# Optimization experiments

Hardware: AMD Instinct MI355X
Metric: run time of the kernel (lower is better)

The kernel has to match this reference:

```python
import jax, jax.numpy as jnp
import numpy as np


def setup_inputs() -> dict:
    key = jax.random.key(0)
    k1, k2, k3 = jax.random.split(key, 3)
    p = 4096
    target = jax.random.normal(k1, (p, p), dtype=jnp.float32)
    source = jax.random.normal(k2, (p, p), dtype=jnp.float32)
    W_beta = jax.random.uniform(k3, (p, p), dtype=jnp.float32)
    return {"target": target, "source": source, "W_beta": W_beta}


def reference(target, source, W_beta):
    # X = target, Y = source (module-level names in the original).
    # denominator inner loop: sum_i X[i] . X[i] == ||X||_F^2 (scalar),
    # recomputed p^2 times in the original; computed once here.
    s = jnp.sum(target * target)
    W = W_beta.sum(axis=1)                       # [p]
    W2 = W * W                                   # [p]
    scale = W2 / (s * W2 + 1.0)                  # [p]
    G = jnp.matmul(source, target.T)             # [p,p], G[i,j] = Y[i] . X[j]
    W_matrix = scale[:, None] * G                # [p,p]
    primary = jnp.matmul(W_matrix, target) - source
    loss = jnp.sqrt(jnp.sum(jnp.square(jnp.matmul(W_beta, primary))))
    return loss, W_matrix
```

## Files before the change

### kernel.cpp

```cpp
#include <hip/hip_runtime.h>
#include <hip/hip_bf16.h>

#define PDIM 4096
#define PPN ((size_t)PDIM * (size_t)PDIM)

typedef __attribute__((ext_vector_type(8))) short bf16x8;
typedef __attribute__((ext_vector_type(4))) float floatx4;
typedef __attribute__((ext_vector_type(8))) int int8v;

__device__ __forceinline__ void load_lds16(const void* g, void* l) {
  __builtin_amdgcn_global_load_lds(
      (const __attribute__((address_space(1))) void*)g,
      (__attribute__((address_space(3))) void*)l, 16, 0, 0);
}

__device__ __forceinline__ unsigned short bf16bits(float f) {
  __hip_bfloat16 h = __float2bfloat16(f);
  return *(unsigned short*)&h;
}

__device__ __forceinline__ unsigned char fp8byte(float v) {
  return (unsigned char)(__builtin_amdgcn_cvt_pk_fp8_f32(v, v, 0, false) & 0xff);
}
__device__ __forceinline__ unsigned int fp8x4(float a, float b, float c, float d) {
  int v = __builtin_amdgcn_cvt_pk_fp8_f32(a, b, 0, false);
  v = __builtin_amdgcn_cvt_pk_fp8_f32(c, d, v, true);
  return (unsigned int)v;
}

__global__ void sumsq(const float4* __restrict__ x, float* __restrict__ acc) {
  float s = 0.f;
  const size_t n4 = PPN / 4;
  for (size_t i = (size_t)blockIdx.x * 256 + threadIdx.x; i < n4;
       i += (size_t)gridDim.x * 256) {
    const float4 v = x[i];
    s += v.x * v.x + v.y * v.y + v.z * v.z + v.w * v.w;
  }
#pragma unroll
  for (int off = 32; off > 0; off >>= 1) s += __shfl_down(s, off);
  __shared__ float ws[4];
  if ((threadIdx.x & 63) == 0) ws[threadIdx.x >> 6] = s;
  __syncthreads();
  if (threadIdx.x == 0) atomicAdd(acc, ws[0] + ws[1] + ws[2] + ws[3]);
}

__global__ void cast_x(const float* __restrict__ src,
                       __hip_bfloat16* __restrict__ dstN,
                       unsigned char* __restrict__ dstT8) {
  __shared__ float tile[64][65];
  const int bx = blockIdx.x * 64, by = blockIdx.y * 64;
  const int tx = threadIdx.x & 15, ty = threadIdx.x >> 4;
#pragma unroll
  for (int r = 0; r < 4; ++r) {
    const int row = ty + r * 16;
    const float4 v = *(const float4*)&src[(size_t)(by + row) * PDIM + bx + tx * 4];
    tile[row][tx * 4 + 0] = v.x;
    tile[row][tx * 4 + 1] = v.y;
    tile[row][tx * 4 + 2] = v.z;
    tile[row][tx * 4 + 3] = v.w;
    ushort4 o;
    o.x = bf16bits(v.x); o.y = bf16bits(v.y); o.z = bf16bits(v.z); o.w = bf16bits(v.w);
    *(ushort4*)&dstN[(size_t)(by + row) * PDIM + bx + tx * 4] = o;
  }
  __syncthreads();
#pragma unroll
  for (int r = 0; r < 4; ++r) {
    const int i = ty + r * 16;
    *(unsigned int*)&dstT8[(size_t)(bx + i) * PDIM + by + tx * 4] =
        fp8x4(tile[tx * 4 + 0][i], tile[tx * 4 + 1][i],
              tile[tx * 4 + 2][i], tile[tx * 4 + 3][i]);
  }
}

__global__ void cast_y(const float* __restrict__ src,
                       __hip_bfloat16* __restrict__ dstN,
                       __hip_bfloat16* __restrict__ dstT) {
  __shared__ float tile[64][65];
  const int bx = blockIdx.x * 64, by = blockIdx.y * 64;
  const int tx = threadIdx.x & 15, ty = threadIdx.x >> 4;
#pragma unroll
  for (int r = 0; r < 4; ++r) {
    const int row = ty + r * 16;
    const float4 v = *(const float4*)&src[(size_t)(by + row) * PDIM + bx + tx * 4];
    tile[row][tx * 4 + 0] = v.x;
    tile[row][tx * 4 + 1] = v.y;
    tile[row][tx * 4 + 2] = v.z;
    tile[row][tx * 4 + 3] = v.w;
    ushort4 o;
    o.x = bf16bits(v.x); o.y = bf16bits(v.y); o.z = bf16bits(v.z); o.w = bf16bits(v.w);
    *(ushort4*)&dstN[(size_t)(by + row) * PDIM + bx + tx * 4] = o;
  }
  __syncthreads();
#pragma unroll
  for (int r = 0; r < 4; ++r) {
    const int i = ty + r * 16;
    ushort4 o;
    o.x = bf16bits(tile[tx * 4 + 0][i]);
    o.y = bf16bits(tile[tx * 4 + 1][i]);
    o.z = bf16bits(tile[tx * 4 + 2][i]);
    o.w = bf16bits(tile[tx * 4 + 3][i]);
    *(ushort4*)&dstT[(size_t)(bx + i) * PDIM + by + tx * 4] = o;
  }
}

__global__ void cast_wb_rows(const float* __restrict__ Wb,
                             unsigned char* __restrict__ Wb8,
                             const float* __restrict__ sAcc,
                             float* __restrict__ scale) {
  const size_t row = blockIdx.x;
  const float4* src = (const float4*)(Wb + row * PDIM);
  unsigned int* dst = (unsigned int*)(Wb8 + row * PDIM);
  float sum = 0.f;
#pragma unroll
  for (int it = 0; it < 4; ++it) {
    const int j = threadIdx.x + it * 256;
    const float4 v = src[j];
    sum += (v.x + v.y) + (v.z + v.w);
    dst[j] = fp8x4(v.x, v.y, v.z, v.w);
  }
#pragma unroll
  for (int off = 32; off > 0; off >>= 1) sum += __shfl_down(sum, off);
  __shared__ float ws[4];
  if ((threadIdx.x & 63) == 0) ws[threadIdx.x >> 6] = sum;
  __syncthreads();
  if (threadIdx.x == 0) {
    const float W = ws[0] + ws[1] + ws[2] + ws[3];
    const float w2 = W * W;
    scale[row] = w2 / ((*sAcc) * w2 + 1.0f);
  }
}

__global__ __launch_bounds__(256)
void gemm_bf16_wm(const __hip_bfloat16* __restrict__ A,
                  const __hip_bfloat16* __restrict__ B,
                  const float* __restrict__ scale,
                  float* __restrict__ outF,
                  unsigned char* __restrict__ Wm8) {
  __shared__ __align__(16) __hip_bfloat16 As[128 * 32];
  __shared__ __align__(16) __hip_bfloat16 Bs[128 * 32];

  const int tid = threadIdx.x;
  const int lane = tid & 63;
  const int wave = tid >> 6;
  const int wm = wave >> 1, wn = wave & 1;

  const size_t rowA0 = (size_t)blockIdx.y * 128;
  const size_t rowB0 = (size_t)blockIdx.x * 128;

  const int c0 = tid, c1 = tid + 256;
  const int r0 = c0 >> 2, r1 = c1 >> 2;
  const int sc0 = (c0 & 3) ^ ((r0 >> 1) & 3);
  const int sc1 = (c1 & 3) ^ ((r1 >> 1) & 3);
  const __hip_bfloat16* gA0 = A + (rowA0 + (size_t)r0) * PDIM + sc0 * 8;
  const __hip_bfloat16* gA1 = A + (rowA0 + (size_t)r1) * PDIM + sc1 * 8;
  const __hip_bfloat16* gB0 = B + (rowB0 + (size_t)r0) * PDIM + sc0 * 8;
  const __hip_bfloat16* gB1 = B + (rowB0 + (size_t)r1) * PDIM + sc1 * 8;

  char* ldsA0 = (char*)As + wave * 1024;
  char* ldsA1 = (char*)As + 4096 + wave * 1024;
  char* ldsB0 = (char*)Bs + wave * 1024;
  char* ldsB1 = (char*)Bs + 4096 + wave * 1024;

  floatx4 acc[4][4] = {};

  const int fr = lane & 15;
  const int kq = lane >> 4;
  const int sw = (fr >> 1) & 3;
  const int ko = (kq ^ sw) * 16;

  for (int kt = 0; kt < PDIM; kt += 32) {
    load_lds16(gA0 + kt, ldsA0);
    load_lds16(gA1 + kt, ldsA1);
    load_lds16(gB0 + kt, ldsB0);
    load_lds16(gB1 + kt, ldsB1);
    __syncthreads();

    bf16x8 af[4], bfr[4];
#pragma unroll
    for (int mi = 0; mi < 4; ++mi)
      af[mi] = *(const bf16x8*)((const char*)As + (wm * 64 + mi * 16 + fr) * 64 + ko);
#pragma unroll
    for (int ni = 0; ni < 4; ++ni)
      bfr[ni] = *(const bf16x8*)((const char*)Bs + (wn * 64 + ni * 16 + fr) * 64 + ko);
#pragma unroll
    for (int mi = 0; mi < 4; ++mi)
#pragma unroll
      for (int ni = 0; ni < 4; ++ni)
        acc[mi][ni] = __builtin_amdgcn_mfma_f32_16x16x32_bf16(
            af[mi], bfr[ni], acc[mi][ni], 0, 0, 0);
    __syncthreads();
  }

  const size_t row0 = rowA0 + wm * 64;
  const size_t col0 = rowB0 + wn * 64;
  const int lr = (lane >> 4) << 2;
  const int lc = lane & 15;

#pragma unroll
  for (int mi = 0; mi < 4; ++mi) {
#pragma unroll
    for (int r = 0; r < 4; ++r) {
      const size_t row = row0 + mi * 16 + lr + r;
      const float sc = scale[row];
#pragma unroll
      for (int ni = 0; ni < 4; ++ni) {
        const size_t col = col0 + ni * 16 + lc;
        const float v = sc * acc[mi][ni][r];
        outF[row * PDIM + col] = v;
        Wm8[row * PDIM + col] = fp8byte(v * 131072.f);
      }
    }
  }
}

template <int MODE>
__global__ __launch_bounds__(256)
void gemm_fp8(const unsigned char* __restrict__ A,
              const unsigned char* __restrict__ B,
              const __hip_bfloat16* __restrict__ sub,
              unsigned char* __restrict__ outP,
              float* __restrict__ lossAcc) {
  __shared__ __align__(16) unsigned char As[128 * 128];
  __shared__ __align__(16) unsigned char Bs[128 * 128];

  const int tid = threadIdx.x;
  const int lane = tid & 63;
  const int wave = tid >> 6;
  const int wm = wave >> 1, wn = wave & 1;

  const size_t rowA0 = (size_t)blockIdx.y * 128;
  const size_t rowB0 = (size_t)blockIdx.x * 128;

  const unsigned char* gA[4];
  const unsigned char* gB[4];
  int ldsOff[4];
#pragma unroll
  for (int m = 0; m < 4; ++m) {
    const int ci = tid + m * 256;
    const int r = ci >> 3, s = ci & 7;
    const int cg = s ^ (r & 7);
    gA[m] = A + (rowA0 + (size_t)r) * PDIM + cg * 16;
    gB[m] = B + (rowB0 + (size_t)r) * PDIM + cg * 16;
    ldsOff[m] = m * 4096 + wave * 1024;
  }

  floatx4 acc[4][4] = {};

  const int fr = lane & 15;
  const int e = fr & 7;
  const int q2 = (lane >> 4) << 1;
  const int offLo = (q2 ^ e) << 4;
  const int offHi = ((q2 + 1) ^ e) << 4;
  const int abase = (wm * 64 + fr) * 128;
  const int bbase = (wn * 64 + fr) * 128;

  for (int kt = 0; kt < PDIM; kt += 128) {
#pragma unroll
    for (int m = 0; m < 4; ++m) load_lds16(gA[m] + kt, (char*)As + ldsOff[m]);
#pragma unroll
    for (int m = 0; m < 4; ++m) load_lds16(gB[m] + kt, (char*)Bs + ldsOff[m]);
    __syncthreads();

    union { int8v v; int4 h[2]; } af[4], bg[4];
#pragma unroll
    for (int mi = 0; mi < 4; ++mi) {
      af[mi].h[0] = *(const int4*)(As + abase + mi * 2048 + offLo);
      af[mi].h[1] = *(const int4*)(As + abase + mi * 2048 + offHi);
    }
#pragma unroll
    for (int ni = 0; ni < 4; ++ni) {
      bg[ni].h[0] = *(const int4*)(Bs + bbase + ni * 2048 + offLo);
      bg[ni].h[1] = *(const int4*)(Bs + bbase + ni * 2048 + offHi);
    }
#pragma unroll
    for (int mi = 0; mi < 4; ++mi)
#pragma unroll
      for (int ni = 0; ni < 4; ++ni)
        acc[mi][ni] = __builtin_amdgcn_mfma_scale_f32_16x16x128_f8f6f4(
            af[mi].v, bg[ni].v, acc[mi][ni],
            0 , 0 , 0, 0x7F7F7F7F, 0, 0x7F7F7F7F);
    __syncthreads();
  }

  const size_t row0 = rowA0 + wm * 64;
  const size_t col0 = rowB0 + wn * 64;
  const int lr = (lane >> 4) << 2;
  const int lc = lane & 15;

  if constexpr (MODE == 2) {
    float tot = 0.f;
#pragma unroll
    for (int mi = 0; mi < 4; ++mi)
#pragma unroll
      for (int ni = 0; ni < 4; ++ni)
#pragma unroll
        for (int r = 0; r < 4; ++r) tot += acc[mi][ni][r] * acc[mi][ni][r];
#pragma unroll
    for (int off = 32; off > 0; off >>= 1) tot += __shfl_down(tot, off);
    __shared__ float ws[4];
    if (lane == 0) ws[wave] = tot;
    __syncthreads();
    if (tid == 0) atomicAdd(lossAcc, ws[0] + ws[1] + ws[2] + ws[3]);
  } else {
    constexpr float INV = 1.f / 131072.f;
#pragma unroll
    for (int mi = 0; mi < 4; ++mi) {
#pragma unroll
      for (int r = 0; r < 4; ++r) {
        const size_t row = row0 + mi * 16 + lr + r;
#pragma unroll
        for (int ni = 0; ni < 4; ++ni) {
          const size_t col = col0 + ni * 16 + lc;
          const float v = acc[mi][ni][r] * INV - __bfloat162float(sub[row * PDIM + col]);
          outP[row * PDIM + col] = fp8byte(v);
        }
      }
    }
  }
}

__global__ void finalize(float* __restrict__ out, const float* __restrict__ acc) {
  if (threadIdx.x == 0) out[0] = sqrtf(*acc);
}

extern "C" void kernel_launch(void* const* d_in, const int* in_sizes, int n_in,
                              void* d_out, int out_size, void* d_ws, size_t ws_size,
                              hipStream_t stream) {
  const float* X  = (const float*)d_in[0];
  const float* Y  = (const float*)d_in[1];
  const float* Wb = (const float*)d_in[2];
  float* out = (float*)d_out;

  __hip_bfloat16* Xb   = (__hip_bfloat16*)d_ws;
  __hip_bfloat16* Yb   = Xb + PPN;
  __hip_bfloat16* YbT  = Yb + PPN;
  unsigned char*  XT8  = (unsigned char*)(YbT + PPN);
  unsigned char*  Wm8  = XT8 + PPN;
  unsigned char*  Wb8  = Wm8 + PPN;
  unsigned char*  PT8  = Wb8 + PPN;
  float* scale   = (float*)(PT8 + PPN);
  float* sAcc    = scale + PDIM;
  float* lossAcc = sAcc + 1;

  hipMemsetAsync(sAcc, 0, 2 * sizeof(float), stream);

  sumsq<<<1024, 256, 0, stream>>>((const float4*)X, sAcc);

  dim3 cgrid(PDIM / 64, PDIM / 64);
  cast_x<<<cgrid, 256, 0, stream>>>(X, Xb, XT8);
  cast_y<<<cgrid, 256, 0, stream>>>(Y, Yb, YbT);
  cast_wb_rows<<<PDIM, 256, 0, stream>>>(Wb, Wb8, sAcc, scale);

  dim3 ggrid(PDIM / 128, PDIM / 128);
  gemm_bf16_wm<<<ggrid, 256, 0, stream>>>(Yb, Xb, scale, out + 1, Wm8);
  gemm_fp8<1><<<ggrid, 256, 0, stream>>>(XT8, Wm8, YbT, PT8, nullptr);
  gemm_fp8<2><<<ggrid, 256, 0, stream>>>(PT8, Wb8, nullptr, nullptr, lossAcc);

  finalize<<<1, 1, 0, stream>>>(out, lossAcc);
}
```

Baseline: 602.9 us.

## Fuse sum-of-squares into X cast and double-buffer bf16 GEMM LDS tiles

Drops the standalone sumsq pass over X. The squared-norm partials are now computed inside cast_x, one per block, and reduced by a small scale kernel, which also computes the per-row scale from row sums written by cast_wb_rows. The bf16 GEMM now uses two LDS buffers so the next K-tile's global-to-LDS load is issued before the current tile's MFMAs. This saves a 64MB read of X and aims to overlap loads with compute, at the cost of a single-block extra launch and double the LDS use in the GEMM.

Measured after the change: 613.7 us. Within noise of the previous version (+1.8%).

```diff
diff --git a/kernel.cpp b/kernel.cpp
--- a/kernel.cpp
+++ b/kernel.cpp
@@ -28,25 +28,47 @@
   return (unsigned int)v;
 }
 
-__global__ void sumsq(const float4* __restrict__ x, float* __restrict__ acc) {
-  float s = 0.f;
-  const size_t n4 = PPN / 4;
-  for (size_t i = (size_t)blockIdx.x * 256 + threadIdx.x; i < n4;
-       i += (size_t)gridDim.x * 256) {
-    const float4 v = x[i];
-    s += v.x * v.x + v.y * v.y + v.z * v.z + v.w * v.w;
-  }
-#pragma unroll
-  for (int off = 32; off > 0; off >>= 1) s += __shfl_down(s, off);
-  __shared__ float ws[4];
-  if ((threadIdx.x & 63) == 0) ws[threadIdx.x >> 6] = s;
-  __syncthreads();
-  if (threadIdx.x == 0) atomicAdd(acc, ws[0] + ws[1] + ws[2] + ws[3]);
-}
-
 __global__ void cast_x(const float* __restrict__ src,
                        __hip_bfloat16* __restrict__ dstN,
-                       unsigned char* __restrict__ dstT8) {
+                       unsigned char* __restrict__ dstT8,
+                       float* __restrict__ partX) {
+  __shared__ float tile[64][65];
+  const int bx = blockIdx.x * 64, by = blockIdx.y * 64;
+  const int tx = threadIdx.x & 15, ty = threadIdx.x >> 4;
+  float lsq = 0.f;
+#pragma unroll
+  for (int r = 0; r < 4; ++r) {
+    const int row = ty + r * 16;
+    const float4 v = *(const float4*)&src[(size_t)(by + row) * PDIM + bx + tx * 4];
+    tile[row][tx * 4 + 0] = v.x;
+    tile[row][tx * 4 + 1] = v.y;
+    tile[row][tx * 4 + 2] = v.z;
+    tile[row][tx * 4 + 3] = v.w;
+    lsq += v.x * v.x + v.y * v.y + v.z * v.z + v.w * v.w;
+    ushort4 o;
+    o.x = bf16bits(v.x); o.y = bf16bits(v.y); o.z = bf16bits(v.z); o.w = bf16bits(v.w);
+    *(ushort4*)&dstN[(size_t)(by + row) * PDIM + bx + tx * 4] = o;
+  }
+  __syncthreads();
+#pragma unroll
+  for (int r = 0; r < 4; ++r) {
+    const int i = ty + r * 16;
+    *(unsigned int*)&dstT8[(size_t)(bx + i) * PDIM + by + tx * 4] =
+        fp8x4(tile[tx * 4 + 0][i], tile[tx * 4 + 1][i],
+              tile[tx * 4 + 2][i], tile[tx * 4 + 3][i]);
+  }
+#pragma unroll
+  for (int off = 32; off > 0; off >>= 1) lsq += __shfl_down(lsq, off);
+  __shared__ float ws[4];
+  if ((threadIdx.x & 63) == 0) ws[threadIdx.x >> 6] = lsq;
+  __syncthreads();
+  if (threadIdx.x == 0)
+    partX[blockIdx.y * 64 + blockIdx.x] = ws[0] + ws[1] + ws[2] + ws[3];
+}
+
+__global__ void cast_y(const float* __restrict__ src,
+                       __hip_bfloat16* __restrict__ dstN,
+                       __hip_bfloat16* __restrict__ dstT) {
   __shared__ float tile[64][65];
   const int bx = blockIdx.x * 64, by = blockIdx.y * 64;
   const int tx = threadIdx.x & 15, ty = threadIdx.x >> 4;
@@ -66,34 +88,6 @@
 #pragma unroll
   for (int r = 0; r < 4; ++r) {
     const int i = ty + r * 16;
-    *(unsigned int*)&dstT8[(size_t)(bx + i) * PDIM + by + tx * 4] =
-        fp8x4(tile[tx * 4 + 0][i], tile[tx * 4 + 1][i],
-              tile[tx * 4 + 2][i], tile[tx * 4 + 3][i]);
-  }
-}
-
-__global__ void cast_y(const float* __restrict__ src,
-                       __hip_bfloat16* __restrict__ dstN,
-                       __hip_bfloat16* __restrict__ dstT) {
-  __shared__ float tile[64][65];
-  const int bx = blockIdx.x * 64, by = blockIdx.y * 64;
-  const int tx = threadIdx.x & 15, ty = threadIdx.x >> 4;
-#pragma unroll
-  for (int r = 0; r < 4; ++r) {
-    const int row = ty + r * 16;
-    const float4 v = *(const float4*)&src[(size_t)(by + row) * PDIM + bx + tx * 4];
-    tile[row][tx * 4 + 0] = v.x;
-    tile[row][tx * 4 + 1] = v.y;
-    tile[row][tx * 4 + 2] = v.z;
-    tile[row][tx * 4 + 3] = v.w;
-    ushort4 o;
-    o.x = bf16bits(v.x); o.y = bf16bits(v.y); o.z = bf16bits(v.z); o.w = bf16bits(v.w);
-    *(ushort4*)&dstN[(size_t)(by + row) * PDIM + bx + tx * 4] = o;
-  }
-  __syncthreads();
-#pragma unroll
-  for (int r = 0; r < 4; ++r) {
-    const int i = ty + r * 16;
     ushort4 o;
     o.x = bf16bits(tile[tx * 4 + 0][i]);
     o.y = bf16bits(tile[tx * 4 + 1][i]);
@@ -105,8 +99,7 @@
 
 __global__ void cast_wb_rows(const float* __restrict__ Wb,
                              unsigned char* __restrict__ Wb8,
-                             const float* __restrict__ sAcc,
-                             float* __restrict__ scale) {
+                             float* __restrict__ Wrow) {
   const size_t row = blockIdx.x;
   const float4* src = (const float4*)(Wb + row * PDIM);
   unsigned int* dst = (unsigned int*)(Wb8 + row * PDIM);
@@ -123,10 +116,24 @@
   __shared__ float ws[4];
   if ((threadIdx.x & 63) == 0) ws[threadIdx.x >> 6] = sum;
   __syncthreads();
-  if (threadIdx.x == 0) {
-    const float W = ws[0] + ws[1] + ws[2] + ws[3];
+  if (threadIdx.x == 0) Wrow[row] = ws[0] + ws[1] + ws[2] + ws[3];
+}
+
+__global__ void scale_k(const float* __restrict__ partX,
+                        const float* __restrict__ Wrow,
+                        float* __restrict__ scale) {
+  float s = 0.f;
+  for (int i = threadIdx.x; i < PDIM; i += 256) s += partX[i];
+#pragma unroll
+  for (int off = 32; off > 0; off >>= 1) s += __shfl_down(s, off);
+  __shared__ float ws[4];
+  if ((threadIdx.x & 63) == 0) ws[threadIdx.x >> 6] = s;
+  __syncthreads();
+  const float st = ws[0] + ws[1] + ws[2] + ws[3];
+  for (int i = threadIdx.x; i < PDIM; i += 256) {
+    const float W = Wrow[i];
     const float w2 = W * W;
-    scale[row] = w2 / ((*sAcc) * w2 + 1.0f);
+    scale[i] = w2 / (st * w2 + 1.0f);
   }
 }
 
@@ -136,8 +143,8 @@
                   const float* __restrict__ scale,
                   float* __restrict__ outF,
                   unsigned char* __restrict__ Wm8) {
-  __shared__ __align__(16) __hip_bfloat16 As[128 * 32];
-  __shared__ __align__(16) __hip_bfloat16 Bs[128 * 32];
+  __shared__ __align__(16) __hip_bfloat16 As[2][128 * 32];
+  __shared__ __align__(16) __hip_bfloat16 Bs[2][128 * 32];
 
   const int tid = threadIdx.x;
   const int lane = tid & 63;
@@ -156,11 +163,6 @@
   const __hip_bfloat16* gB0 = B + (rowB0 + (size_t)r0) * PDIM + sc0 * 8;
   const __hip_bfloat16* gB1 = B + (rowB0 + (size_t)r1) * PDIM + sc1 * 8;
 
-  char* ldsA0 = (char*)As + wave * 1024;
-  char* ldsA1 = (char*)As + 4096 + wave * 1024;
-  char* ldsB0 = (char*)Bs + wave * 1024;
-  char* ldsB1 = (char*)Bs + 4096 + wave * 1024;
-
   floatx4 acc[4][4] = {};
 
   const int fr = lane & 15;
@@ -168,28 +170,44 @@
   const int sw = (fr >> 1) & 3;
   const int ko = (kq ^ sw) * 16;
 
-  for (int kt = 0; kt < PDIM; kt += 32) {
-    load_lds16(gA0 + kt, ldsA0);
-    load_lds16(gA1 + kt, ldsA1);
-    load_lds16(gB0 + kt, ldsB0);
-    load_lds16(gB1 + kt, ldsB1);
-    __syncthreads();
-
+  auto stage = [&](int b, int kt) {
+    char* a = (char*)As[b] + wave * 1024;
+    char* bb = (char*)Bs[b] + wave * 1024;
+    load_lds16(gA0 + kt, a);
+    load_lds16(gA1 + kt, a + 4096);
+    load_lds16(gB0 + kt, bb);
+    load_lds16(gB1 + kt, bb + 4096);
+  };
+  auto compute = [&](int b) {
     bf16x8 af[4], bfr[4];
 #pragma unroll
     for (int mi = 0; mi < 4; ++mi)
-      af[mi] = *(const bf16x8*)((const char*)As + (wm * 64 + mi * 16 + fr) * 64 + ko);
+      af[mi] = *(const bf16x8*)((const char*)As[b] + (wm * 64 + mi * 16 + fr) * 64 + ko);
 #pragma unroll
     for (int ni = 0; ni < 4; ++ni)
-      bfr[ni] = *(const bf16x8*)((const char*)Bs + (wn * 64 + ni * 16 + fr) * 64 + ko);
+      bfr[ni] = *(const bf16x8*)((const char*)Bs[b] + (wn * 64 + ni * 16 + fr) * 64 + ko);
 #pragma unroll
     for (int mi = 0; mi < 4; ++mi)
 #pragma unroll
       for (int ni = 0; ni < 4; ++ni)
         acc[mi][ni] = __builtin_amdgcn_mfma_f32_16x16x32_bf16(
             af[mi], bfr[ni], acc[mi][ni], 0, 0, 0);
-    __syncthreads();
-  }
+  };
+
+  stage(0, 0);
+  __syncthreads();
+  stage(1, 32);
+  for (int kt = 0; kt < PDIM - 64; kt += 64) {
+    compute(0);
+    __syncthreads();
+    stage(0, kt + 64);
+    compute(1);
+    __syncthreads();
+    stage(1, kt + 96);
+  }
+  compute(0);
+  __syncthreads();
+  compute(1);
 
   const size_t row0 = rowA0 + wm * 64;
   const size_t col0 = rowB0 + wn * 64;
@@ -339,17 +357,17 @@
   unsigned char*  Wb8  = Wm8 + PPN;
   unsigned char*  PT8  = Wb8 + PPN;
   float* scale   = (float*)(PT8 + PPN);
-  float* sAcc    = scale + PDIM;
-  float* lossAcc = sAcc + 1;
-
-  hipMemsetAsync(sAcc, 0, 2 * sizeof(float), stream);
-
-  sumsq<<<1024, 256, 0, stream>>>((const float4*)X, sAcc);
+  float* partX   = scale + PDIM;
+  float* Wrow    = partX + PDIM;
+  float* lossAcc = Wrow + PDIM;
+
+  hipMemsetAsync(lossAcc, 0, sizeof(float), stream);
 
   dim3 cgrid(PDIM / 64, PDIM / 64);
-  cast_x<<<cgrid, 256, 0, stream>>>(X, Xb, XT8);
+  cast_x<<<cgrid, 256, 0, stream>>>(X, Xb, XT8, partX);
   cast_y<<<cgrid, 256, 0, stream>>>(Y, Yb, YbT);
-  cast_wb_rows<<<PDIM, 256, 0, stream>>>(Wb, Wb8, sAcc, scale);
+  cast_wb_rows<<<PDIM, 256, 0, stream>>>(Wb, Wb8, Wrow);
+  scale_k<<<1, 256, 0, stream>>>(partX, Wrow, scale);
 
   dim3 ggrid(PDIM / 128, PDIM / 128);
   gemm_bf16_wm<<<ggrid, 256, 0, stream>>>(Yb, Xb, scale, out + 1, Wm8);
```
